# Performance work log

Hardware: AMD Instinct MI355X
Metric: run time of the kernel (lower is better)

Reference implementation:

```python
import jax, jax.numpy as jnp
import numpy as np

E, D, I, T = 8, 4096, 1024, 32768  # experts, model dim, dim//4, total packed tokens


def setup_inputs() -> dict:
    key = jax.random.key(0)
    k1, k2, k3, k4 = jax.random.split(key, 4)
    x = jax.random.normal(k1, (T, D), dtype=jnp.float32)
    # trunc_normal(std=0.02) approximated by scaled normal for the reference
    w1 = jax.random.normal(k2, (E, D, I), dtype=jnp.float32) * 0.02
    w2 = jax.random.normal(k3, (E, I, D), dtype=jnp.float32) * 0.02
    w3 = jax.random.normal(k4, (E, D, I), dtype=jnp.float32) * 0.02
    # tokens split evenly across experts; sum == T
    num_tokens_per_expert = jnp.full((E,), T // E, dtype=jnp.int32)
    return {"x": x, "w1": w1, "w2": w2, "w3": w3,
            "num_tokens_per_expert": num_tokens_per_expert}


def reference(x, w1, w2, w3, num_tokens_per_expert):
    # bf16 compute, cast back to input dtype (matches ops.gmm path in torch code)
    g = num_tokens_per_expert.astype(jnp.int32)
    xb = x.astype(jnp.bfloat16)
    w1b = w1.astype(jnp.bfloat16)
    w2b = w2.astype(jnp.bfloat16)
    w3b = w3.astype(jnp.bfloat16)
    # grouped GEMM: rows of x are grouped by expert per g
    x1 = jax.lax.ragged_dot(xb, w1b, g)          # [T, I]
    x3 = jax.lax.ragged_dot(xb, w3b, g)          # [T, I]
    h = jax.nn.silu(x1) * x3                      # SwiGLU
    out = jax.lax.ragged_dot(h, w2b, g)           # [T, D]
    return out.astype(x.dtype)
```

## Files before the change

### kernel.cpp

```cpp
#include <hip/hip_runtime.h>
#include <hip/hip_bf16.h>

typedef __attribute__((ext_vector_type(8))) short bf16x8;
typedef __attribute__((ext_vector_type(4))) float f32x4;

#define SBAR() __builtin_amdgcn_sched_barrier(0)
#define WBAR() __builtin_amdgcn_s_barrier()

template<int N> __device__ __forceinline__ void vmcw() {
  if constexpr (N >= 12)     asm volatile("s_waitcnt vmcnt(12)" ::: "memory");
  else if constexpr (N == 8) asm volatile("s_waitcnt vmcnt(8)" ::: "memory");
  else if constexpr (N == 4) asm volatile("s_waitcnt vmcnt(4)" ::: "memory");
  else                       asm volatile("s_waitcnt vmcnt(0)" ::: "memory");
}

__device__ __forceinline__ ushort f2bf(float f) {
  union { float f; unsigned u; } v; v.f = f;
  unsigned r = v.u + 0x7fffu + ((v.u >> 16) & 1u);
  return (ushort)(r >> 16);
}

__device__ __forceinline__ void gld_lds16(const ushort* gsrc, ushort* lds) {
  __builtin_amdgcn_global_load_lds((const __attribute__((address_space(1))) void*)gsrc,
                                   (__attribute__((address_space(3))) void*)lds, 16, 0, 0);
}

__device__ __forceinline__ f32x4 MF(bf16x8 a, bf16x8 b, f32x4 c) {
  return __builtin_amdgcn_mfma_f32_16x16x32_bf16(a, b, c, 0, 0, 0);
}

__device__ __forceinline__ void xcd_map(int bid, int CT, int& r, int& c) {
  const int xcd = bid & 7, j = bid >> 3;
  r = xcd + 8 * (j / CT);
  c = j % CT;
}

__device__ __forceinline__ int expert_of(const int* g, int E, int m0) {
  int e = 0, base = 0;
  while (e < E - 1 && m0 >= base + g[e]) { base += g[e]; ++e; }
  return e;
}

__global__ __launch_bounds__(256) void k_pack_x(
    const float* __restrict__ x, ushort* __restrict__ xb, int D) {
  __shared__ ushort sm[256][66];
  const int kt = blockIdx.x;
  const int rt = blockIdx.y;
  const int t = threadIdx.x;
  const int c0 = kt * 64;
  const size_t r0 = (size_t)rt * 256;
#pragma unroll
  for (int p = 0; p < 16; ++p) {
    const int row = p * 16 + (t >> 4);
    const float4 v = *reinterpret_cast<const float4*>(x + (r0 + row) * D + c0 + (t & 15) * 4);
    ushort4 u; u.x = f2bf(v.x); u.y = f2bf(v.y); u.z = f2bf(v.z); u.w = f2bf(v.w);
    *reinterpret_cast<ushort4*>(&sm[row][(t & 15) * 4]) = u;
  }
  __syncthreads();
  ushort* outp = xb + ((size_t)rt * (D >> 6) + kt) * 16384;
#pragma unroll
  for (int p = 0; p < 8; ++p) {
    ushort u[8];
#pragma unroll
    for (int j = 0; j < 8; ++j) u[j] = sm[t][p * 8 + j];
    *reinterpret_cast<uint4*>(outp + p * 2048 + t * 8) = *reinterpret_cast<uint4*>(u);
  }
}

__global__ __launch_bounds__(256) void k_pack_w(
    const float* __restrict__ w, ushort* __restrict__ wp, int R, int C, int rbShift) {
  __shared__ ushort sm[64][66];
  const int e = blockIdx.z;
  const size_t mat = (size_t)R * C;
  const float* s = w + (size_t)e * mat;
  ushort* d = wp + (size_t)e * mat;
  const int c0 = blockIdx.x * 64;
  const int r0 = blockIdx.y * 64;
  const int t = threadIdx.x;
#pragma unroll
  for (int p = 0; p < 4; ++p) {
    const int r = p * 16 + (t >> 4);
    const float4 v = *reinterpret_cast<const float4*>(s + (size_t)(r0 + r) * C + c0 + (t & 15) * 4);
    ushort4 u; u.x = f2bf(v.x); u.y = f2bf(v.y); u.z = f2bf(v.z); u.w = f2bf(v.w);
    *reinterpret_cast<ushort4*>(&sm[r][(t & 15) * 4]) = u;
  }
  __syncthreads();
  const int RB = 1 << rbShift;
  const size_t tilebase = ((size_t)(c0 >> rbShift) * (R >> 6) + (r0 >> 6)) * ((size_t)RB * 64);
  const int nbase = c0 & (RB - 1);
#pragma unroll
  for (int p = 0; p < 2; ++p) {
    const int uu = p * 256 + t;
    const int kc = uu >> 6;
    const int rr = uu & 63;
    ushort u[8];
#pragma unroll
    for (int j = 0; j < 8; ++j) u[j] = sm[kc * 8 + j][rr];
    *reinterpret_cast<uint4*>(d + tilebase + (size_t)kc * (RB * 8) + (size_t)(nbase + rr) * 8) =
        *reinterpret_cast<uint4*>(u);
  }
}

template<bool PF, int C1, int C2>
__device__ __forceinline__ void g1_tile(
    ushort* B, const ushort* nA, const ushort* nB1, const ushort* nB3,
    int sto, int aoff, int b1off, int b3off,
    f32x4 (&acc1)[8][2], f32x4 (&acc3)[8][2]) {
  bf16x8 af[4], b1f[2], b3f[2];
  SBAR();
#pragma unroll
  for (int mi = 0; mi < 4; ++mi) af[mi] = *(const bf16x8*)&B[aoff + mi * 128];
  b1f[0] = *(const bf16x8*)&B[b1off];       b1f[1] = *(const bf16x8*)&B[b1off + 128];
  b3f[0] = *(const bf16x8*)&B[b3off];       b3f[1] = *(const bf16x8*)&B[b3off + 128];
  SBAR(); WBAR(); SBAR();
  __builtin_amdgcn_s_setprio(1);
#pragma unroll
  for (int mi = 0; mi < 4; ++mi)
#pragma unroll
    for (int ni = 0; ni < 2; ++ni) {
      acc1[mi][ni] = MF(af[mi], b1f[ni], acc1[mi][ni]);
      acc3[mi][ni] = MF(af[mi], b3f[ni], acc3[mi][ni]);
    }
  __builtin_amdgcn_s_setprio(0);
  SBAR(); WBAR();
  SBAR();
#pragma unroll
  for (int mi = 0; mi < 4; ++mi) af[mi] = *(const bf16x8*)&B[aoff + (mi + 4) * 128];
  SBAR(); WBAR(); SBAR();
  if (PF) {
    gld_lds16(nA + sto,         B + sto);
    gld_lds16(nA + 4096 + sto,  B + 4096 + sto);
    gld_lds16(nB1 + sto,        B + 16384 + sto);
    gld_lds16(nB3 + sto,        B + 24576 + sto);
  }
  __builtin_amdgcn_s_setprio(1);
#pragma unroll
  for (int mi = 0; mi < 4; ++mi)
#pragma unroll
    for (int ni = 0; ni < 2; ++ni) {
      acc1[mi + 4][ni] = MF(af[mi], b1f[ni], acc1[mi + 4][ni]);
      acc3[mi + 4][ni] = MF(af[mi], b3f[ni], acc3[mi + 4][ni]);
    }
  __builtin_amdgcn_s_setprio(0);
  SBAR();
  vmcw<C1>();
  WBAR();
  SBAR();
#pragma unroll
  for (int mi = 0; mi < 4; ++mi) af[mi] = *(const bf16x8*)&B[aoff + 8192 + mi * 128];
  b1f[0] = *(const bf16x8*)&B[b1off + 4096]; b1f[1] = *(const bf16x8*)&B[b1off + 4096 + 128];
  b3f[0] = *(const bf16x8*)&B[b3off + 4096]; b3f[1] = *(const bf16x8*)&B[b3off + 4096 + 128];
  SBAR(); WBAR(); SBAR();
  __builtin_amdgcn_s_setprio(1);
#pragma unroll
  for (int mi = 0; mi < 4; ++mi)
#pragma unroll
    for (int ni = 0; ni < 2; ++ni) {
      acc1[mi][ni] = MF(af[mi], b1f[ni], acc1[mi][ni]);
      acc3[mi][ni] = MF(af[mi], b3f[ni], acc3[mi][ni]);
    }
  __builtin_amdgcn_s_setprio(0);
  SBAR(); WBAR();
  SBAR();
#pragma unroll
  for (int mi = 0; mi < 4; ++mi) af[mi] = *(const bf16x8*)&B[aoff + 8192 + (mi + 4) * 128];
  SBAR(); WBAR(); SBAR();
  if (PF) {
    gld_lds16(nA + 8192 + sto,   B + 8192 + sto);
    gld_lds16(nA + 12288 + sto,  B + 12288 + sto);
    gld_lds16(nB1 + 4096 + sto,  B + 20480 + sto);
    gld_lds16(nB3 + 4096 + sto,  B + 28672 + sto);
  }
  __builtin_amdgcn_s_setprio(1);
#pragma unroll
  for (int mi = 0; mi < 4; ++mi)
#pragma unroll
    for (int ni = 0; ni < 2; ++ni) {
      acc1[mi + 4][ni] = MF(af[mi], b1f[ni], acc1[mi + 4][ni]);
      acc3[mi + 4][ni] = MF(af[mi], b3f[ni], acc3[mi + 4][ni]);
    }
  __builtin_amdgcn_s_setprio(0);
  SBAR();
  vmcw<C2>();
  WBAR();
}

__global__ __launch_bounds__(512, 2) void k_gemm1_8p(
    const ushort* __restrict__ xb, const ushort* __restrict__ w1p,
    const ushort* __restrict__ w3p, const int* __restrict__ g,
    ushort* __restrict__ h, int T, int D, int I, int E) {
  __shared__ ushort lds[2][32768];

  const int CT = I >> 7;
  int r, c; xcd_map(blockIdx.x, CT, r, c);
  const int m0 = r << 8, n0 = c << 7;
  const int e = expert_of(g, E, m0);

  const int tid = threadIdx.x;
  const int lane = tid & 63, wave = tid >> 6;
  const int wr = wave >> 2, wc = wave & 3;
  const int l15 = lane & 15, l16 = lane >> 4;

  const int KT = D >> 6;
  const ushort* pA  = xb  + (size_t)r * (D >> 6) * 16384;
  const ushort* pB1 = w1p + (size_t)e * I * D + (size_t)c * (D >> 6) * 8192;
  const ushort* pB3 = w3p + (size_t)e * I * D + (size_t)c * (D >> 6) * 8192;

  const int sto = tid * 8;
  const int aoff  = l16 * 2048 + (wr * 128 + l15) * 8;
  const int b1off = 16384 + l16 * 1024 + (wc * 32 + l15) * 8;
  const int b3off = b1off + 8192;

  const f32x4 zero = {0.f, 0.f, 0.f, 0.f};
  f32x4 acc1[8][2], acc3[8][2];
#pragma unroll
  for (int mi = 0; mi < 8; ++mi)
#pragma unroll
    for (int ni = 0; ni < 2; ++ni) { acc1[mi][ni] = zero; acc3[mi][ni] = zero; }

  {
    ushort* L0 = lds[0]; ushort* L1 = lds[1];
    gld_lds16(pA + sto,          L0 + sto);
    gld_lds16(pA + 4096 + sto,   L0 + 4096 + sto);
    gld_lds16(pB1 + sto,         L0 + 16384 + sto);
    gld_lds16(pB3 + sto,         L0 + 24576 + sto);
    gld_lds16(pA + 8192 + sto,   L0 + 8192 + sto);
    gld_lds16(pA + 12288 + sto,  L0 + 12288 + sto);
    gld_lds16(pB1 + 4096 + sto,  L0 + 20480 + sto);
    gld_lds16(pB3 + 4096 + sto,  L0 + 28672 + sto);
    gld_lds16(pA + 16384 + sto,         L1 + sto);
    gld_lds16(pA + 16384 + 4096 + sto,  L1 + 4096 + sto);
    gld_lds16(pB1 + 8192 + sto,         L1 + 16384 + sto);
    gld_lds16(pB3 + 8192 + sto,         L1 + 24576 + sto);
    gld_lds16(pA + 16384 + 8192 + sto,  L1 + 8192 + sto);
    gld_lds16(pA + 16384 + 12288 + sto, L1 + 12288 + sto);
    gld_lds16(pB1 + 8192 + 4096 + sto,  L1 + 20480 + sto);
    gld_lds16(pB3 + 8192 + 4096 + sto,  L1 + 28672 + sto);
  }
  vmcw<12>(); WBAR(); SBAR();

  int t = 0;
  for (; t < KT - 2; ++t)
    g1_tile<true, 12, 12>(lds[t & 1], pA + (size_t)(t + 2) * 16384,
                          pB1 + (size_t)(t + 2) * 8192, pB3 + (size_t)(t + 2) * 8192,
                          sto, aoff, b1off, b3off, acc1, acc3);
  g1_tile<false, 8, 4>(lds[t & 1], pA, pB1, pB3, sto, aoff, b1off, b3off, acc1, acc3);
  ++t;
  g1_tile<false, 0, 0>(lds[t & 1], pA, pB1, pB3, sto, aoff, b1off, b3off, acc1, acc3);

#pragma unroll
  for (int mi = 0; mi < 8; ++mi)
#pragma unroll
    for (int ni = 0; ni < 2; ++ni)
#pragma unroll
      for (int rr = 0; rr < 4; ++rr) {
        const float v1 = acc1[mi][ni][rr];
        const float v3 = acc3[mi][ni][rr];
        const float sv = v1 / (1.f + __expf(-v1));
        const int row = m0 + wr * 128 + mi * 16 + l16 * 4 + rr;
        const int col = n0 + wc * 32 + ni * 16 + l15;
        const size_t off = ((size_t)(row >> 8) * (I >> 6) + (col >> 6)) * 16384 +
                           ((col >> 3) & 7) * 2048 + (row & 255) * 8 + (col & 7);
        h[off] = f2bf(sv * v3);
      }
}

template<bool PF, int C1, int C2>
__device__ __forceinline__ void g2_tile(
    ushort* B, const ushort* nA, const ushort* nB,
    int sto, int aoff, int boff, f32x4 (&acc)[8][4]) {
  bf16x8 af[4], bf[4];
  SBAR();
#pragma unroll
  for (int mi = 0; mi < 4; ++mi) af[mi] = *(const bf16x8*)&B[aoff + mi * 128];
#pragma unroll
  for (int ni = 0; ni < 4; ++ni) bf[ni] = *(const bf16x8*)&B[boff + ni * 128];
  SBAR(); WBAR(); SBAR();
  __builtin_amdgcn_s_setprio(1);
#pragma unroll
  for (int mi = 0; mi < 4; ++mi)
#pragma unroll
    for (int ni = 0; ni < 4; ++ni) acc[mi][ni] = MF(af[mi], bf[ni], acc[mi][ni]);
  __builtin_amdgcn_s_setprio(0);
  SBAR(); WBAR();
  SBAR();
#pragma unroll
  for (int mi = 0; mi < 4; ++mi) af[mi] = *(const bf16x8*)&B[aoff + (mi + 4) * 128];
  SBAR(); WBAR(); SBAR();
  if (PF) {
    gld_lds16(nA + sto,         B + sto);
    gld_lds16(nA + 4096 + sto,  B + 4096 + sto);
    gld_lds16(nB + sto,         B + 16384 + sto);
    gld_lds16(nB + 4096 + sto,  B + 20480 + sto);
  }
  __builtin_amdgcn_s_setprio(1);
#pragma unroll
  for (int mi = 0; mi < 4; ++mi)
#pragma unroll
    for (int ni = 0; ni < 4; ++ni) acc[mi + 4][ni] = MF(af[mi], bf[ni], acc[mi + 4][ni]);
  __builtin_amdgcn_s_setprio(0);
  SBAR();
  vmcw<C1>();
  WBAR();
  SBAR();
#pragma unroll
  for (int mi = 0; mi < 4; ++mi) af[mi] = *(const bf16x8*)&B[aoff + 8192 + mi * 128];
#pragma unroll
  for (int ni = 0; ni < 4; ++ni) bf[ni] = *(const bf16x8*)&B[boff + 8192 + ni * 128];
  SBAR(); WBAR(); SBAR();
  __builtin_amdgcn_s_setprio(1);
#pragma unroll
  for (int mi = 0; mi < 4; ++mi)
#pragma unroll
    for (int ni = 0; ni < 4; ++ni) acc[mi][ni] = MF(af[mi], bf[ni], acc[mi][ni]);
  __builtin_amdgcn_s_setprio(0);
  SBAR(); WBAR();
  SBAR();
#pragma unroll
  for (int mi = 0; mi < 4; ++mi) af[mi] = *(const bf16x8*)&B[aoff + 8192 + (mi + 4) * 128];
  SBAR(); WBAR(); SBAR();
  if (PF) {
    gld_lds16(nA + 8192 + sto,   B + 8192 + sto);
    gld_lds16(nA + 12288 + sto,  B + 12288 + sto);
    gld_lds16(nB + 8192 + sto,   B + 24576 + sto);
    gld_lds16(nB + 12288 + sto,  B + 28672 + sto);
  }
  __builtin_amdgcn_s_setprio(1);
#pragma unroll
  for (int mi = 0; mi < 4; ++mi)
#pragma unroll
    for (int ni = 0; ni < 4; ++ni) acc[mi + 4][ni] = MF(af[mi], bf[ni], acc[mi + 4][ni]);
  __builtin_amdgcn_s_setprio(0);
  SBAR();
  vmcw<C2>();
  WBAR();
}

__global__ __launch_bounds__(512, 2) void k_gemm2_8p(
    const ushort* __restrict__ h, const ushort* __restrict__ w2p,
    const int* __restrict__ g, float* __restrict__ out,
    int T, int D, int I, int E) {
  __shared__ ushort lds[2][32768];

  const int CT = D >> 8;
  int r, cb; xcd_map(blockIdx.x, CT, r, cb);
  const int m0 = r << 8, n0 = cb << 8;
  const int e = expert_of(g, E, m0);

  const int tid = threadIdx.x;
  const int lane = tid & 63, wave = tid >> 6;
  const int wr = wave >> 2, wc = wave & 3;
  const int l15 = lane & 15, l16 = lane >> 4;

  const int KT = I >> 6;
  const ushort* pA = h   + (size_t)r * (I >> 6) * 16384;
  const ushort* pB = w2p + (size_t)e * D * I + (size_t)cb * (I >> 6) * 16384;

  const int sto = tid * 8;
  const int aoff = l16 * 2048 + (wr * 128 + l15) * 8;
  const int boff = 16384 + l16 * 2048 + (wc * 64 + l15) * 8;

  const f32x4 zero = {0.f, 0.f, 0.f, 0.f};
  f32x4 acc[8][4];
#pragma unroll
  for (int mi = 0; mi < 8; ++mi)
#pragma unroll
    for (int ni = 0; ni < 4; ++ni) acc[mi][ni] = zero;

  {
    ushort* L0 = lds[0]; ushort* L1 = lds[1];
    gld_lds16(pA + sto,          L0 + sto);
    gld_lds16(pA + 4096 + sto,   L0 + 4096 + sto);
    gld_lds16(pB + sto,          L0 + 16384 + sto);
    gld_lds16(pB + 4096 + sto,   L0 + 20480 + sto);
    gld_lds16(pA + 8192 + sto,   L0 + 8192 + sto);
    gld_lds16(pA + 12288 + sto,  L0 + 12288 + sto);
    gld_lds16(pB + 8192 + sto,   L0 + 24576 + sto);
    gld_lds16(pB + 12288 + sto,  L0 + 28672 + sto);
    gld_lds16(pA + 16384 + sto,          L1 + sto);
    gld_lds16(pA + 16384 + 4096 + sto,   L1 + 4096 + sto);
    gld_lds16(pB + 16384 + sto,          L1 + 16384 + sto);
    gld_lds16(pB + 16384 + 4096 + sto,   L1 + 20480 + sto);
    gld_lds16(pA + 16384 + 8192 + sto,   L1 + 8192 + sto);
    gld_lds16(pA + 16384 + 12288 + sto,  L1 + 12288 + sto);
    gld_lds16(pB + 16384 + 8192 + sto,   L1 + 24576 + sto);
    gld_lds16(pB + 16384 + 12288 + sto,  L1 + 28672 + sto);
  }
  vmcw<12>(); WBAR(); SBAR();

  int t = 0;
  for (; t < KT - 2; ++t)
    g2_tile<true, 12, 12>(lds[t & 1], pA + (size_t)(t + 2) * 16384,
                          pB + (size_t)(t + 2) * 16384, sto, aoff, boff, acc);
  g2_tile<false, 8, 4>(lds[t & 1], pA, pB, sto, aoff, boff, acc);
  ++t;
  g2_tile<false, 0, 0>(lds[t & 1], pA, pB, sto, aoff, boff, acc);

#pragma unroll
  for (int mi = 0; mi < 8; ++mi)
#pragma unroll
    for (int ni = 0; ni < 4; ++ni)
#pragma unroll
      for (int rr = 0; rr < 4; ++rr) {
        const int row = m0 + wr * 128 + mi * 16 + l16 * 4 + rr;
        const int col = n0 + wc * 64 + ni * 16 + l15;
        out[(size_t)row * D + col] = acc[mi][ni][rr];
      }
}

extern "C" void kernel_launch(void* const* d_in, const int* in_sizes, int n_in,
                              void* d_out, int out_size, void* d_ws, size_t ws_size,
                              hipStream_t stream) {
  const float* x  = (const float*)d_in[0];
  const float* w1 = (const float*)d_in[1];
  const float* w2 = (const float*)d_in[2];
  const float* w3 = (const float*)d_in[3];
  const int*   g  = (const int*)d_in[4];

  const int E = in_sizes[4];
  const int D = 4096;
  const int I = 1024;
  const int T = in_sizes[0] / D;

  const size_t szW = (size_t)E * D * I * sizeof(ushort);
  const size_t szH = (size_t)T * I * sizeof(ushort);
  const size_t szX = (size_t)T * D * sizeof(ushort);
  const size_t need = 2 * szW + szH + szX;
  if (ws_size < need) return;

  char* ws = (char*)d_ws;
  ushort* w1p = (ushort*)ws;
  ushort* w3p = (ushort*)(ws + szW);
  ushort* h   = (ushort*)(ws + 2 * szW);
  ushort* xb  = (ushort*)(ws + 2 * szW + szH);
  ushort* w2p = w1p;

  float* out = (float*)d_out;

  k_pack_w<<<dim3(I / 64, D / 64, E), 256, 0, stream>>>(w1, w1p, D, I, 7);
  k_pack_w<<<dim3(I / 64, D / 64, E), 256, 0, stream>>>(w3, w3p, D, I, 7);
  k_pack_x<<<dim3(D / 64, T / 256), 256, 0, stream>>>(x, xb, D);

  k_gemm1_8p<<<dim3((T / 256) * (I / 128)), 512, 0, stream>>>(xb, w1p, w3p, g, h, T, D, I, E);

  k_pack_w<<<dim3(D / 64, I / 64, E), 256, 0, stream>>>(w2, w2p, I, D, 8);

  k_gemm2_8p<<<dim3((T / 256) * (D / 256)), 512, 0, stream>>>(h, w2p, g, out, T, D, I, E);
}
```

Baseline: 1.053 ms.

## Fuse x fp32-to-bf16 conversion into gemm1 A-tile loading

```diff
diff --git a/kernel.cpp b/kernel.cpp
--- a/kernel.cpp
+++ b/kernel.cpp
@@ -6,12 +6,15 @@
 
 #define SBAR() __builtin_amdgcn_sched_barrier(0)
 #define WBAR() __builtin_amdgcn_s_barrier()
+#define LGKM0() asm volatile("s_waitcnt lgkmcnt(0)" ::: "memory")
 
 template<int N> __device__ __forceinline__ void vmcw() {
-  if constexpr (N >= 12)     asm volatile("s_waitcnt vmcnt(12)" ::: "memory");
-  else if constexpr (N == 8) asm volatile("s_waitcnt vmcnt(8)" ::: "memory");
-  else if constexpr (N == 4) asm volatile("s_waitcnt vmcnt(4)" ::: "memory");
-  else                       asm volatile("s_waitcnt vmcnt(0)" ::: "memory");
+  if constexpr (N == 12)      asm volatile("s_waitcnt vmcnt(12)" ::: "memory");
+  else if constexpr (N == 10) asm volatile("s_waitcnt vmcnt(10)" ::: "memory");
+  else if constexpr (N == 8)  asm volatile("s_waitcnt vmcnt(8)" ::: "memory");
+  else if constexpr (N == 4)  asm volatile("s_waitcnt vmcnt(4)" ::: "memory");
+  else if constexpr (N == 2)  asm volatile("s_waitcnt vmcnt(2)" ::: "memory");
+  else                        asm volatile("s_waitcnt vmcnt(0)" ::: "memory");
 }
 
 __device__ __forceinline__ ushort f2bf(float f) {
@@ -20,6 +23,12 @@
   return (ushort)(r >> 16);
 }
 
+__device__ __forceinline__ unsigned cvtpk(float lo, float hi) {
+  unsigned r;
+  asm volatile("v_cvt_pk_bf16_f32 %0, %1, %2" : "=v"(r) : "v"(lo), "v"(hi));
+  return r;
+}
+
 __device__ __forceinline__ void gld_lds16(const ushort* gsrc, ushort* lds) {
   __builtin_amdgcn_global_load_lds((const __attribute__((address_space(1))) void*)gsrc,
                                    (__attribute__((address_space(3))) void*)lds, 16, 0, 0);
@@ -41,34 +50,55 @@
   return e;
 }
 
-__global__ __launch_bounds__(256) void k_pack_x(
-    const float* __restrict__ x, ushort* __restrict__ xb, int D) {
-  __shared__ ushort sm[256][66];
-  const int kt = blockIdx.x;
-  const int rt = blockIdx.y;
+__device__ __forceinline__ void store_A(ushort* L, int awr, const float4 (&av)[8]) {
+#pragma unroll
+  for (int cc = 0; cc < 4; ++cc) {
+    uint4 w;
+    w.x = cvtpk(av[2 * cc].x,     av[2 * cc].y);
+    w.y = cvtpk(av[2 * cc].z,     av[2 * cc].w);
+    w.z = cvtpk(av[2 * cc + 1].x, av[2 * cc + 1].y);
+    w.w = cvtpk(av[2 * cc + 1].z, av[2 * cc + 1].w);
+    *reinterpret_cast<uint4*>(&L[awr + cc * 2048]) = w;
+  }
+}
+
+__global__ __launch_bounds__(256) void k_pack_w13(
+    const float* __restrict__ w1, const float* __restrict__ w3,
+    ushort* __restrict__ w1p, ushort* __restrict__ w3p, int R, int C) {
+  __shared__ ushort sm[64][66];
+  const int bz = blockIdx.z;
+  const int e = bz >> 1;
+  const size_t mat = (size_t)R * C;
+  const float* s = ((bz & 1) ? w3 : w1) + (size_t)e * mat;
+  ushort* d = ((bz & 1) ? w3p : w1p) + (size_t)e * mat;
+  const int c0 = blockIdx.x * 64;
+  const int r0 = blockIdx.y * 64;
   const int t = threadIdx.x;
-  const int c0 = kt * 64;
-  const size_t r0 = (size_t)rt * 256;
-#pragma unroll
-  for (int p = 0; p < 16; ++p) {
-    const int row = p * 16 + (t >> 4);
-    const float4 v = *reinterpret_cast<const float4*>(x + (r0 + row) * D + c0 + (t & 15) * 4);
+#pragma unroll
+  for (int p = 0; p < 4; ++p) {
+    const int r = p * 16 + (t >> 4);
+    const float4 v = *reinterpret_cast<const float4*>(s + (size_t)(r0 + r) * C + c0 + (t & 15) * 4);
     ushort4 u; u.x = f2bf(v.x); u.y = f2bf(v.y); u.z = f2bf(v.z); u.w = f2bf(v.w);
-    *reinterpret_cast<ushort4*>(&sm[row][(t & 15) * 4]) = u;
+    *reinterpret_cast<ushort4*>(&sm[r][(t & 15) * 4]) = u;
   }
   __syncthreads();
-  ushort* outp = xb + ((size_t)rt * (D >> 6) + kt) * 16384;
-#pragma unroll
-  for (int p = 0; p < 8; ++p) {
+  const size_t tilebase = ((size_t)(c0 >> 7) * (R >> 6) + (r0 >> 6)) * 8192;
+  const int nbase = c0 & 127;
+#pragma unroll
+  for (int p = 0; p < 2; ++p) {
+    const int uu = p * 256 + t;
+    const int kc = uu >> 6;
+    const int rr = uu & 63;
     ushort u[8];
 #pragma unroll
-    for (int j = 0; j < 8; ++j) u[j] = sm[t][p * 8 + j];
-    *reinterpret_cast<uint4*>(outp + p * 2048 + t * 8) = *reinterpret_cast<uint4*>(u);
-  }
-}
-
-__global__ __launch_bounds__(256) void k_pack_w(
-    const float* __restrict__ w, ushort* __restrict__ wp, int R, int C, int rbShift) {
+    for (int j = 0; j < 8; ++j) u[j] = sm[kc * 8 + j][rr];
+    *reinterpret_cast<uint4*>(d + tilebase + (size_t)kc * 1024 + (size_t)(nbase + rr) * 8) =
+        *reinterpret_cast<uint4*>(u);
+  }
+}
+
+__global__ __launch_bounds__(256) void k_pack_w2(
+    const float* __restrict__ w, ushort* __restrict__ wp, int R, int C) {
   __shared__ ushort sm[64][66];
   const int e = blockIdx.z;
   const size_t mat = (size_t)R * C;
@@ -85,9 +115,8 @@
     *reinterpret_cast<ushort4*>(&sm[r][(t & 15) * 4]) = u;
   }
   __syncthreads();
-  const int RB = 1 << rbShift;
-  const size_t tilebase = ((size_t)(c0 >> rbShift) * (R >> 6) + (r0 >> 6)) * ((size_t)RB * 64);
-  const int nbase = c0 & (RB - 1);
+  const size_t tilebase = ((size_t)(c0 >> 8) * (R >> 6) + (r0 >> 6)) * 16384;
+  const int nbase = c0 & 255;
 #pragma unroll
   for (int p = 0; p < 2; ++p) {
     const int uu = p * 256 + t;
@@ -96,22 +125,28 @@
     ushort u[8];
 #pragma unroll
     for (int j = 0; j < 8; ++j) u[j] = sm[kc * 8 + j][rr];
-    *reinterpret_cast<uint4*>(d + tilebase + (size_t)kc * (RB * 8) + (size_t)(nbase + rr) * 8) =
+    *reinterpret_cast<uint4*>(d + tilebase + (size_t)kc * 2048 + (size_t)(nbase + rr) * 8) =
         *reinterpret_cast<uint4*>(u);
   }
 }
 
-template<bool PF, int C1, int C2>
+template<bool PF, int CP2>
 __device__ __forceinline__ void g1_tile(
-    ushort* B, const ushort* nA, const ushort* nB1, const ushort* nB3,
-    int sto, int aoff, int b1off, int b3off,
+    ushort* B, ushort* N,
+    const float* xnext, const ushort* nB1, const ushort* nB3,
+    int sto, int awr, int aoff, int b1off, int b3off,
     f32x4 (&acc1)[8][2], f32x4 (&acc3)[8][2]) {
   bf16x8 af[4], b1f[2], b3f[2];
+  float4 av[8];
   SBAR();
 #pragma unroll
   for (int mi = 0; mi < 4; ++mi) af[mi] = *(const bf16x8*)&B[aoff + mi * 128];
   b1f[0] = *(const bf16x8*)&B[b1off];       b1f[1] = *(const bf16x8*)&B[b1off + 128];
   b3f[0] = *(const bf16x8*)&B[b3off];       b3f[1] = *(const bf16x8*)&B[b3off + 128];
+  if (PF) {
+#pragma unroll
+    for (int q = 0; q < 8; ++q) av[q] = *reinterpret_cast<const float4*>(xnext + q * 4);
+  }
   SBAR(); WBAR(); SBAR();
   __builtin_amdgcn_s_setprio(1);
 #pragma unroll
@@ -126,13 +161,11 @@
   SBAR();
 #pragma unroll
   for (int mi = 0; mi < 4; ++mi) af[mi] = *(const bf16x8*)&B[aoff + (mi + 4) * 128];
-  SBAR(); WBAR(); SBAR();
-  if (PF) {
-    gld_lds16(nA + sto,         B + sto);
-    gld_lds16(nA + 4096 + sto,  B + 4096 + sto);
-    gld_lds16(nB1 + sto,        B + 16384 + sto);
-    gld_lds16(nB3 + sto,        B + 24576 + sto);
-  }
+  if (PF) {
+    gld_lds16(nB1 + sto, N + 16384 + sto);
+    gld_lds16(nB3 + sto, N + 24576 + sto);
+  }
+  SBAR(); WBAR(); SBAR();
   __builtin_amdgcn_s_setprio(1);
 #pragma unroll
   for (int mi = 0; mi < 4; ++mi)
@@ -143,7 +176,7 @@
     }
   __builtin_amdgcn_s_setprio(0);
   SBAR();
-  vmcw<C1>();
+  vmcw<CP2>();
   WBAR();
   SBAR();
 #pragma unroll
@@ -166,10 +199,10 @@
   for (int mi = 0; mi < 4; ++mi) af[mi] = *(const bf16x8*)&B[aoff + 8192 + (mi + 4) * 128];
   SBAR(); WBAR(); SBAR();
   if (PF) {
-    gld_lds16(nA + 8192 + sto,   B + 8192 + sto);
-    gld_lds16(nA + 12288 + sto,  B + 12288 + sto);
-    gld_lds16(nB1 + 4096 + sto,  B + 20480 + sto);
-    gld_lds16(nB3 + 4096 + sto,  B + 28672 + sto);
+    vmcw<2>();
+    store_A(N, awr, av);
+    gld_lds16(nB1 + 4096 + sto, N + 20480 + sto);
+    gld_lds16(nB3 + 4096 + sto, N + 28672 + sto);
   }
   __builtin_amdgcn_s_setprio(1);
 #pragma unroll
@@ -181,12 +214,15 @@
     }
   __builtin_amdgcn_s_setprio(0);
   SBAR();
-  vmcw<C2>();
+  if (PF) {
+    LGKM0();
+    vmcw<2>();
+  }
   WBAR();
 }
 
 __global__ __launch_bounds__(512, 2) void k_gemm1_8p(
-    const ushort* __restrict__ xb, const ushort* __restrict__ w1p,
+    const float* __restrict__ x, const ushort* __restrict__ w1p,
     const ushort* __restrict__ w3p, const int* __restrict__ g,
     ushort* __restrict__ h, int T, int D, int I, int E) {
   __shared__ ushort lds[2][32768];
@@ -202,7 +238,6 @@
   const int l15 = lane & 15, l16 = lane >> 4;
 
   const int KT = D >> 6;
-  const ushort* pA  = xb  + (size_t)r * (D >> 6) * 16384;
   const ushort* pB1 = w1p + (size_t)e * I * D + (size_t)c * (D >> 6) * 8192;
   const ushort* pB3 = w3p + (size_t)e * I * D + (size_t)c * (D >> 6) * 8192;
 
@@ -211,6 +246,11 @@
   const int b1off = 16384 + l16 * 1024 + (wc * 32 + l15) * 8;
   const int b3off = b1off + 8192;
 
+  const int arow = tid >> 1;
+  const int ahalf = tid & 1;
+  const float* xptr = x + (size_t)(m0 + arow) * D + ahalf * 32;
+  const int awr = ahalf * 8192 + arow * 8;
+
   const f32x4 zero = {0.f, 0.f, 0.f, 0.f};
   f32x4 acc1[8][2], acc3[8][2];
 #pragma unroll
@@ -219,34 +259,29 @@
     for (int ni = 0; ni < 2; ++ni) { acc1[mi][ni] = zero; acc3[mi][ni] = zero; }
 
   {
-    ushort* L0 = lds[0]; ushort* L1 = lds[1];
-    gld_lds16(pA + sto,          L0 + sto);
-    gld_lds16(pA + 4096 + sto,   L0 + 4096 + sto);
-    gld_lds16(pB1 + sto,         L0 + 16384 + sto);
-    gld_lds16(pB3 + sto,         L0 + 24576 + sto);
-    gld_lds16(pA + 8192 + sto,   L0 + 8192 + sto);
-    gld_lds16(pA + 12288 + sto,  L0 + 12288 + sto);
-    gld_lds16(pB1 + 4096 + sto,  L0 + 20480 + sto);
-    gld_lds16(pB3 + 4096 + sto,  L0 + 28672 + sto);
-    gld_lds16(pA + 16384 + sto,         L1 + sto);
-    gld_lds16(pA + 16384 + 4096 + sto,  L1 + 4096 + sto);
-    gld_lds16(pB1 + 8192 + sto,         L1 + 16384 + sto);
-    gld_lds16(pB3 + 8192 + sto,         L1 + 24576 + sto);
-    gld_lds16(pA + 16384 + 8192 + sto,  L1 + 8192 + sto);
-    gld_lds16(pA + 16384 + 12288 + sto, L1 + 12288 + sto);
-    gld_lds16(pB1 + 8192 + 4096 + sto,  L1 + 20480 + sto);
-    gld_lds16(pB3 + 8192 + 4096 + sto,  L1 + 28672 + sto);
-  }
-  vmcw<12>(); WBAR(); SBAR();
+    ushort* L0 = lds[0];
+    float4 pav[8];
+#pragma unroll
+    for (int q = 0; q < 8; ++q) pav[q] = *reinterpret_cast<const float4*>(xptr + q * 4);
+    gld_lds16(pB1 + sto,        L0 + 16384 + sto);
+    gld_lds16(pB3 + sto,        L0 + 24576 + sto);
+    gld_lds16(pB1 + 4096 + sto, L0 + 20480 + sto);
+    gld_lds16(pB3 + 4096 + sto, L0 + 28672 + sto);
+    vmcw<4>();
+    store_A(L0, awr, pav);
+    LGKM0();
+    vmcw<2>();
+  }
+  WBAR(); SBAR();
 
   int t = 0;
-  for (; t < KT - 2; ++t)
-    g1_tile<true, 12, 12>(lds[t & 1], pA + (size_t)(t + 2) * 16384,
-                          pB1 + (size_t)(t + 2) * 8192, pB3 + (size_t)(t + 2) * 8192,
-                          sto, aoff, b1off, b3off, acc1, acc3);
-  g1_tile<false, 8, 4>(lds[t & 1], pA, pB1, pB3, sto, aoff, b1off, b3off, acc1, acc3);
-  ++t;
-  g1_tile<false, 0, 0>(lds[t & 1], pA, pB1, pB3, sto, aoff, b1off, b3off, acc1, acc3);
+  for (; t < KT - 1; ++t)
+    g1_tile<true, 10>(lds[t & 1], lds[(t + 1) & 1],
+                      xptr + (size_t)(t + 1) * 64,
+                      pB1 + (size_t)(t + 1) * 8192, pB3 + (size_t)(t + 1) * 8192,
+                      sto, awr, aoff, b1off, b3off, acc1, acc3);
+  g1_tile<false, 0>(lds[t & 1], lds[t & 1], xptr, pB1, pB3,
+                    sto, awr, aoff, b1off, b3off, acc1, acc3);
 
 #pragma unroll
   for (int mi = 0; mi < 8; ++mi)
@@ -424,26 +459,20 @@
 
   const size_t szW = (size_t)E * D * I * sizeof(ushort);
   const size_t szH = (size_t)T * I * sizeof(ushort);
-  const size_t szX = (size_t)T * D * sizeof(ushort);
-  const size_t need = 2 * szW + szH + szX;
+  const size_t need = 3 * szW + szH;
   if (ws_size < need) return;
 
   char* ws = (char*)d_ws;
   ushort* w1p = (ushort*)ws;
   ushort* w3p = (ushort*)(ws + szW);
-  ushort* h   = (ushort*)(ws + 2 * szW);
-  ushort* xb  = (ushort*)(ws + 2 * szW + szH);
-  ushort* w2p = w1p;
+  ushort* w2p = (ushort*)(ws + 2 * szW);
+  ushort* h   = (ushort*)(ws + 3 * szW);
 
   float* out = (float*)d_out;
 
-  k_pack_w<<<dim3(I / 64, D / 64, E), 256, 0, stream>>>(w1, w1p, D, I, 7);
-  k_pack_w<<<dim3(I / 64, D / 64, E), 256, 0, stream>>>(w3, w3p, D, I, 7);
-  k_pack_x<<<dim3(D / 64, T / 256), 256, 0, stream>>>(x, xb, D);
-
-  k_gemm1_8p<<<dim3((T / 256) * (I / 128)), 512, 0, stream>>>(xb, w1p, w3p, g, h, T, D, I, E);
-
-  k_pack_w<<<dim3(D / 64, I / 64, E), 256, 0, stream>>>(w2, w2p, I, D, 8);
-
+  k_pack_w13<<<dim3(I / 64, D / 64, 2 * E), 256, 0, stream>>>(w1, w3, w1p, w3p, D, I);
+  k_pack_w2<<<dim3(D / 64, I / 64, E), 256, 0, stream>>>(w2, w2p, I, D);
+
+  k_gemm1_8p<<<dim3((T / 256) * (I / 128)), 512, 0, stream>>>(x, w1p, w3p, g, h, T, D, I, E);
   k_gemm2_8p<<<dim3((T / 256) * (D / 256)), 512, 0, stream>>>(h, w2p, g, out, T, D, I, E);
 }
```

Result: slower. 1.334 ms (+26.7%).
